# Performance work log

Hardware: AMD Instinct MI355X
Metric: run time of the kernel (lower is better)

Reference implementation:

```python
import jax, jax.numpy as jnp
import numpy as np

B, C, O, H, W, K, PAD = 8, 256, 256, 56, 56, 3, 1
KK = K * K


def setup_inputs() -> dict:
    key = jax.random.key(0)
    k1, k2, k3, k4 = jax.random.split(key, 4)
    x = jax.random.normal(k1, (B, C, H, W), jnp.float32)
    # offset conv params (original zero-inits; small random used so sampling is off-grid)
    w_off = jax.random.normal(k2, (2 * KK, C, K, K), jnp.float32) * 0.01
    b_off = jnp.zeros((2 * KK,), jnp.float32)
    # deformable conv weight/bias (torchvision DeformConv2d default has bias)
    w_dcn = jax.random.normal(k3, (O, C, K, K), jnp.float32) * (1.0 / np.sqrt(C * KK))
    b_dcn = jax.random.normal(k4, (O,), jnp.float32) * 0.01
    return dict(x=x, w_off=w_off, b_off=b_off, w_dcn=w_dcn, b_dcn=b_dcn)


def _conv3x3(x, w, b):
    y = jax.lax.conv_general_dilated(
        x, w, window_strides=(1, 1), padding=((PAD, PAD), (PAD, PAD)),
        dimension_numbers=('NCHW', 'OIHW', 'NCHW'))
    return y + b[None, :, None, None]


def _deform_sample(x, py, px):
    """Zero-padded bilinear gather of x[B,C,H,W] at (py,px)[B,KK,H,W] -> [B,C,KK,H,W]."""
    xf = x.reshape(B, C, H * W)
    y0 = jnp.floor(py)
    x0 = jnp.floor(px)
    fy = py - y0
    fx = px - x0
    val = 0.0
    for dy, dx, wgt in ((0, 0, (1 - fy) * (1 - fx)),
                        (0, 1, (1 - fy) * fx),
                        (1, 0, fy * (1 - fx)),
                        (1, 1, fy * fx)):
        yc = y0 + dy
        xc = x0 + dx
        ok = (yc >= 0) & (yc < H) & (xc >= 0) & (xc < W)  # zero-padding outside
        yi = jnp.clip(yc, 0, H - 1).astype(jnp.int32)
        xi = jnp.clip(xc, 0, W - 1).astype(jnp.int32)
        idx = (yi * W + xi).reshape(B, 1, KK * H * W)  # broadcast over channel dim
        g = jnp.take_along_axis(xf, idx, axis=2).reshape(B, C, KK, H, W)
        val = val + (wgt * ok)[:, None] * g
    return val


def reference(x, w_off, b_off, w_dcn, b_dcn):
    # 1) predict per-pixel offsets: [B, 2*K*K, H, W], torchvision layout (dy,dx) pairs
    off = _conv3x3(x, w_off, b_off)
    dy = off[:, 0::2]  # [B, KK, H, W]
    dx = off[:, 1::2]
    # 2) sampling grid: base pixel + kernel tap offset + learned offset
    ky = (jnp.arange(KK) // K - PAD).astype(jnp.float32)
    kx = (jnp.arange(KK) % K - PAD).astype(jnp.float32)
    hgrid = jnp.arange(H, dtype=jnp.float32)
    wgrid = jnp.arange(W, dtype=jnp.float32)
    py = hgrid[None, None, :, None] + ky[None, :, None, None] + dy
    px = wgrid[None, None, None, :] + kx[None, :, None, None] + dx
    # 3) bilinear gather + weighted accumulation over (c, kernel tap)
    val = _deform_sample(x, py, px)  # [B, C, KK, H, W]
    out = jnp.einsum('bckhw,ock->bohw', val, w_dcn.reshape(O, C, KK))
    return out + b_dcn[None, :, None, None]
```

## Files before the change

### kernel.cpp

```cpp
#include <hip/hip_runtime.h>

#define B_  8
#define C_  256
#define O_  256
#define H_  56
#define W_  56
#define HW_ 3136
#define KK_ 9
#define CK_ 2304
#define NKC 72

typedef __bf16    bf16x8 __attribute__((ext_vector_type(8)));
typedef float     f32x4  __attribute__((ext_vector_type(4)));

__device__ __forceinline__ int swz4(int r) { return (r & 3) ^ ((r >> 2) & 3); }

__device__ __forceinline__ float blo(unsigned u) {
    return __builtin_bit_cast(float, u << 16);
}
__device__ __forceinline__ float bhi(unsigned u) {
    return __builtin_bit_cast(float, u & 0xffff0000u);
}
__device__ __forceinline__ unsigned pkbf(float lo, float hi) {
    unsigned short a = __builtin_bit_cast(unsigned short, (__bf16)lo);
    unsigned short b = __builtin_bit_cast(unsigned short, (__bf16)hi);
    return (unsigned)a | ((unsigned)b << 16);
}

__device__ __forceinline__ uint4 bilin4(uint4 c00, uint4 c01, uint4 c10, uint4 c11,
                                        float4 wg) {
    uint4 o;
    float lo_, hi_;
    lo_ = wg.x*blo(c00.x) + wg.y*blo(c01.x) + wg.z*blo(c10.x) + wg.w*blo(c11.x);
    hi_ = wg.x*bhi(c00.x) + wg.y*bhi(c01.x) + wg.z*bhi(c10.x) + wg.w*bhi(c11.x);
    o.x = pkbf(lo_, hi_);
    lo_ = wg.x*blo(c00.y) + wg.y*blo(c01.y) + wg.z*blo(c10.y) + wg.w*blo(c11.y);
    hi_ = wg.x*bhi(c00.y) + wg.y*bhi(c01.y) + wg.z*bhi(c10.y) + wg.w*bhi(c11.y);
    o.y = pkbf(lo_, hi_);
    lo_ = wg.x*blo(c00.z) + wg.y*blo(c01.z) + wg.z*blo(c10.z) + wg.w*blo(c11.z);
    hi_ = wg.x*bhi(c00.z) + wg.y*bhi(c01.z) + wg.z*bhi(c10.z) + wg.w*bhi(c11.z);
    o.z = pkbf(lo_, hi_);
    lo_ = wg.x*blo(c00.w) + wg.y*blo(c01.w) + wg.z*blo(c10.w) + wg.w*blo(c11.w);
    hi_ = wg.x*bhi(c00.w) + wg.y*bhi(c01.w) + wg.z*bhi(c10.w) + wg.w*bhi(c11.w);
    o.w = pkbf(lo_, hi_);
    return o;
}

__global__ __launch_bounds__(256) void k_buildA(const float* __restrict__ w,
                                                unsigned short* __restrict__ wA) {
    int d  = blockIdx.x * 256 + threadIdx.x;
    int kc = d >> 13;
    int rd = d & 8191;
    int m  = rd >> 5;
    int pos = rd & 31;
    int q  = (pos >> 3) ^ swz4(m);
    int kl = q * 8 + (pos & 7);
    int gk = kc * 32 + kl;
    int tap = gk >> 8, c = gk & 255;
    __bf16 v = (__bf16)w[m * CK_ + c * KK_ + tap];
    wA[d] = __builtin_bit_cast(unsigned short, v);
}

__global__ __launch_bounds__(256) void k_transx(const float* __restrict__ x,
                                                unsigned short* __restrict__ xT) {
    __shared__ float s[64][65];
    int bt   = blockIdx.x;
    int c64  = bt & 3;
    int hw64 = (bt >> 2) % 49;
    int b    = bt / 196;
    int tx = threadIdx.x & 63;
    int ty = threadIdx.x >> 6;
#pragma unroll
    for (int i = 0; i < 16; ++i)
        s[i * 4 + ty][tx] =
            x[((size_t)(b * 256 + c64 * 64 + i * 4 + ty)) * HW_ + hw64 * 64 + tx];
    __syncthreads();
#pragma unroll
    for (int i = 0; i < 16; ++i) {
        float v = s[tx][i * 4 + ty];
        xT[((size_t)b * HW_ + hw64 * 64 + i * 4 + ty) * 256 + c64 * 64 + tx] =
            __builtin_bit_cast(unsigned short, (__bf16)v);
    }
}

__global__ __launch_bounds__(512) void k_offc1(const float* __restrict__ x,
                                               const float* __restrict__ w_off,
                                               float* __restrict__ part) {
    __shared__ float partial[8][64][18];
    int t  = threadIdx.x;
    int p  = t & 63;
    int cg = __builtin_amdgcn_readfirstlane(t >> 6);
    int orig = blockIdx.x;
    int blk  = (orig & 7) * 196 + (orig >> 3);
    int sl   = blk & 3;
    int un   = blk >> 2;
    int b    = un / 49;
    int pos0 = (un % 49) * 64;
    int pos  = pos0 + p;
    int h = pos / W_;
    int w = pos % W_;
    const float* xb = x + (size_t)b * C_ * HW_;

    float acc[18];
#pragma unroll
    for (int i = 0; i < 18; ++i) acc[i] = 0.f;

    for (int cc = 0; cc < 8; ++cc) {
        int c = sl * 64 + cg * 8 + cc;
        const float* xp = xb + c * HW_;
        float v[9];
#pragma unroll
        for (int dh = -1; dh <= 1; ++dh)
#pragma unroll
            for (int dw = -1; dw <= 1; ++dw) {
                int hh = h + dh, ww = w + dw;
                bool ok = (hh >= 0) & (hh < H_) & (ww >= 0) & (ww < W_);
                v[(dh + 1) * 3 + dw + 1] = ok ? xp[hh * W_ + ww] : 0.f;
            }
        const float* wc = w_off + c * KK_;
#pragma unroll
        for (int oc = 0; oc < 18; ++oc) {
            const float* wr = wc + oc * CK_;
#pragma unroll
            for (int k = 0; k < KK_; ++k)
                acc[oc] = fmaf(v[k], wr[k], acc[oc]);
        }
    }
#pragma unroll
    for (int oc = 0; oc < 18; ++oc) partial[cg][p][oc] = acc[oc];
    __syncthreads();

    float* po = part + (size_t)sl * (B_ * 18 * HW_);
    for (int e = t; e < 64 * 18; e += 512) {
        int oc = e >> 6;
        int pp = e & 63;
        float s = 0.f;
#pragma unroll
        for (int g = 0; g < 8; ++g) s += partial[g][pp][oc];
        po[((size_t)b * 18 + oc) * HW_ + pos0 + pp] = s;
    }
}

__global__ __launch_bounds__(256) void k_offc2(const float* __restrict__ part,
                                               const float* __restrict__ b_off,
                                               float* __restrict__ off) {
    int i = blockIdx.x * 256 + threadIdx.x;
    const int NP = B_ * 18 * HW_;
    int oc = (i / HW_) % 18;
    off[i] = part[i] + part[i + NP] + part[i + 2 * NP] + part[i + 3 * NP]
           + b_off[oc];
}

template<bool ISSUEC, bool ISSUEA, bool PROD, bool RELOAD>
__device__ __forceinline__ void fstage(
    int s, int chNext,
    const char* xb, const char* gA0,
    __bf16 (*s_b)[2048],
    int (*s_id)[64][4], float (*s_w)[64][4],
    int4& id, float4& wg,
    bf16x8 (&afUse)[4], bf16x8 (&afFill)[4],
    int aoffBase,
    int n, int tc, int sc, int lid, int quad, int swz,
    f32x4 (&acc)[4][4]) {

    if (RELOAD) {
        id = *(const int4*)s_id[(s + 1) >> 3][n];
        wg = *(const float4*)s_w[(s + 1) >> 3][n];
    }
    uint4 c0, c1, c2, c3;
    if (ISSUEC) {
        const char* p = xb + chNext * 64 + tc * 16;
        c0 = *(const uint4*)(p + id.x);
        c1 = *(const uint4*)(p + id.y);
        c2 = *(const uint4*)(p + id.z);
        c3 = *(const uint4*)(p + id.w);
    }
    if (ISSUEA) {
        const char* ga = gA0 + (size_t)(s + 1) * 16384 + aoffBase;
        afFill[0] = *(const bf16x8*)(ga);
        afFill[1] = *(const bf16x8*)(ga + 1024);
        afFill[2] = *(const bf16x8*)(ga + 2048);
        afFill[3] = *(const bf16x8*)(ga + 3072);
    }

    const bf16x8* pb = (const bf16x8*)s_b[s & 1];
    bf16x8 bv[4];
#pragma unroll
    for (int ni = 0; ni < 4; ++ni)
        bv[ni] = pb[(ni * 16 + lid) * 4 + (quad ^ swz)];

    __builtin_amdgcn_s_setprio(1);
#pragma unroll
    for (int mi = 0; mi < 4; ++mi)
#pragma unroll
        for (int ni = 0; ni < 4; ++ni)
            acc[mi][ni] = __builtin_amdgcn_mfma_f32_16x16x32_bf16(
                afUse[mi], bv[ni], acc[mi][ni], 0, 0, 0);
    __builtin_amdgcn_s_setprio(0);

    if (PROD) {
        uint4 o = bilin4(c0, c1, c2, c3, wg);
        *(uint4*)((char*)s_b[(s & 1) ^ 1] + n * 64 + sc * 16) = o;
    }
    asm volatile("s_waitcnt lgkmcnt(0)" ::: "memory");
    __builtin_amdgcn_s_barrier();
    __builtin_amdgcn_sched_barrier(0);
}

__global__ __launch_bounds__(256, 2) void k_fused(
    const unsigned short* __restrict__ xT,
    const float* __restrict__ off,
    const __bf16* __restrict__ wA,
    const float* __restrict__ b_dcn,
    float* __restrict__ out) {

    __shared__ __bf16 s_b[2][2048];
    __shared__ int    s_id[KK_][64][4];
    __shared__ float  s_w [KK_][64][4];

    int bid  = blockIdx.x;
    int g    = (bid & 7) * 49 + (bid >> 3);
    int b    = g / 49;
    int pos0 = (g % 49) * 64;
    int t    = threadIdx.x;
    int lane = t & 63;
    int wv   = t >> 6;
    int lid  = lane & 15;
    int quad = lane >> 4;
    int swz  = swz4(lid);

    for (int e = t; e < KK_ * 64; e += 256) {
        int k = e >> 6, n = e & 63;
        int pos = pos0 + n;
        int h = pos / W_, w = pos % W_;
        float dy = off[((size_t)b * 18 + 2 * k) * HW_ + pos];
        float dx = off[((size_t)b * 18 + 2 * k + 1) * HW_ + pos];
        float py = (float)(h + k / 3 - 1) + dy;
        float px = (float)(w + k % 3 - 1) + dx;
        float y0f = floorf(py), x0f = floorf(px);
        float fy = py - y0f, fx = px - x0f;
        int y0 = (int)y0f, x0 = (int)x0f;
        int y1 = y0 + 1,   x1 = x0 + 1;
        float oy0 = (y0 >= 0 && y0 < H_) ? 1.f : 0.f;
        float oy1 = (y1 >= 0 && y1 < H_) ? 1.f : 0.f;
        float ox0 = (x0 >= 0 && x0 < W_) ? 1.f : 0.f;
        float ox1 = (x1 >= 0 && x1 < W_) ? 1.f : 0.f;
        int y0c = min(max(y0, 0), H_ - 1), y1c = min(max(y1, 0), H_ - 1);
        int x0c = min(max(x0, 0), W_ - 1), x1c = min(max(x1, 0), W_ - 1);
        s_id[k][n][0] = (y0c * W_ + x0c) * 512;
        s_id[k][n][1] = (y0c * W_ + x1c) * 512;
        s_id[k][n][2] = (y1c * W_ + x0c) * 512;
        s_id[k][n][3] = (y1c * W_ + x1c) * 512;
        s_w[k][n][0] = (1.f - fy) * (1.f - fx) * oy0 * ox0;
        s_w[k][n][1] = (1.f - fy) * fx         * oy0 * ox1;
        s_w[k][n][2] = fy * (1.f - fx)         * oy1 * ox0;
        s_w[k][n][3] = fy * fx                 * oy1 * ox1;
    }
    __syncthreads();

    int n  = t >> 2;
    int tc = t & 3;
    int sc = tc ^ swz4(n);
    const char* xb  = (const char*)(xT + (size_t)b * HW_ * 256);
    const char* gA0 = (const char*)wA;
    int aoffBase = (wv * 64 + lid) * 64 + (quad ^ swz) * 16;

    f32x4 acc[4][4];
#pragma unroll
    for (int mi = 0; mi < 4; ++mi)
#pragma unroll
        for (int ni = 0; ni < 4; ++ni)
            acc[mi][ni] = (f32x4)(0.f);

    int4   id = *(const int4*)s_id[0][n];
    float4 wg = *(const float4*)s_w[0][n];
    bf16x8 afA[4], afB[4];

    {
        const char* p0 = xb + tc * 16;
        uint4 c0 = *(const uint4*)(p0 + id.x);
        uint4 c1 = *(const uint4*)(p0 + id.y);
        uint4 c2 = *(const uint4*)(p0 + id.z);
        uint4 c3 = *(const uint4*)(p0 + id.w);
        const char* ga = gA0 + aoffBase;
        afA[0] = *(const bf16x8*)(ga);
        afA[1] = *(const bf16x8*)(ga + 1024);
        afA[2] = *(const bf16x8*)(ga + 2048);
        afA[3] = *(const bf16x8*)(ga + 3072);
        uint4 o = bilin4(c0, c1, c2, c3, wg);
        *(uint4*)((char*)s_b[0] + n * 64 + sc * 16) = o;
    }
    asm volatile("s_waitcnt lgkmcnt(0)" ::: "memory");
    __builtin_amdgcn_s_barrier();
    __builtin_amdgcn_sched_barrier(0);

    for (int tap = 0; tap < 8; ++tap) {
        int s0 = tap * 8;
        fstage<true, true, true, false>(s0 + 0, 1, xb, gA0, s_b, s_id, s_w, id, wg, afA, afB, aoffBase, n, tc, sc, lid, quad, swz, acc);
        fstage<true, true, true, false>(s0 + 1, 2, xb, gA0, s_b, s_id, s_w, id, wg, afB, afA, aoffBase, n, tc, sc, lid, quad, swz, acc);
        fstage<true, true, true, false>(s0 + 2, 3, xb, gA0, s_b, s_id, s_w, id, wg, afA, afB, aoffBase, n, tc, sc, lid, quad, swz, acc);
        fstage<true, true, true, false>(s0 + 3, 4, xb, gA0, s_b, s_id, s_w, id, wg, afB, afA, aoffBase, n, tc, sc, lid, quad, swz, acc);
        fstage<true, true, true, false>(s0 + 4, 5, xb, gA0, s_b, s_id, s_w, id, wg, afA, afB, aoffBase, n, tc, sc, lid, quad, swz, acc);
        fstage<true, true, true, false>(s0 + 5, 6, xb, gA0, s_b, s_id, s_w, id, wg, afB, afA, aoffBase, n, tc, sc, lid, quad, swz, acc);
        fstage<true, true, true, false>(s0 + 6, 7, xb, gA0, s_b, s_id, s_w, id, wg, afA, afB, aoffBase, n, tc, sc, lid, quad, swz, acc);
        fstage<true, true, true, true >(s0 + 7, 0, xb, gA0, s_b, s_id, s_w, id, wg, afB, afA, aoffBase, n, tc, sc, lid, quad, swz, acc);
    }
    fstage<true,  true,  true,  false>(64, 1, xb, gA0, s_b, s_id, s_w, id, wg, afA, afB, aoffBase, n, tc, sc, lid, quad, swz, acc);
    fstage<true,  true,  true,  false>(65, 2, xb, gA0, s_b, s_id, s_w, id, wg, afB, afA, aoffBase, n, tc, sc, lid, quad, swz, acc);
    fstage<true,  true,  true,  false>(66, 3, xb, gA0, s_b, s_id, s_w, id, wg, afA, afB, aoffBase, n, tc, sc, lid, quad, swz, acc);
    fstage<true,  true,  true,  false>(67, 4, xb, gA0, s_b, s_id, s_w, id, wg, afB, afA, aoffBase, n, tc, sc, lid, quad, swz, acc);
    fstage<true,  true,  true,  false>(68, 5, xb, gA0, s_b, s_id, s_w, id, wg, afA, afB, aoffBase, n, tc, sc, lid, quad, swz, acc);
    fstage<true,  true,  true,  false>(69, 6, xb, gA0, s_b, s_id, s_w, id, wg, afB, afA, aoffBase, n, tc, sc, lid, quad, swz, acc);
    fstage<true,  true,  true,  false>(70, 7, xb, gA0, s_b, s_id, s_w, id, wg, afA, afB, aoffBase, n, tc, sc, lid, quad, swz, acc);
    fstage<false, false, false, false>(71, 0, xb, gA0, s_b, s_id, s_w, id, wg, afB, afA, aoffBase, n, tc, sc, lid, quad, swz, acc);

#pragma unroll
    for (int mi = 0; mi < 4; ++mi) {
#pragma unroll
        for (int r = 0; r < 4; ++r) {
            int m = wv * 64 + mi * 16 + quad * 4 + r;
            float bias = b_dcn[m];
            float* po = out + ((size_t)b * O_ + m) * HW_ + pos0 + lid;
#pragma unroll
            for (int ni = 0; ni < 4; ++ni)
                po[ni * 16] = acc[mi][ni][r] + bias;
        }
    }
}

extern "C" void kernel_launch(void* const* d_in, const int* in_sizes, int n_in,
                              void* d_out, int out_size, void* d_ws, size_t ws_size,
                              hipStream_t stream) {
    const float* x     = (const float*)d_in[0];
    const float* w_off = (const float*)d_in[1];
    const float* b_off = (const float*)d_in[2];
    const float* w_dcn = (const float*)d_in[3];
    const float* b_dcn = (const float*)d_in[4];
    float* out = (float*)d_out;

    const size_t offBytes  = (size_t)451584 * 4;
    const size_t wABytes   = (size_t)589824 * 2;
    const size_t xTBytes   = (size_t)B_ * HW_ * 256 * 2;
    float*          off  = (float*)d_ws;
    unsigned short* wA   = (unsigned short*)((char*)d_ws + offBytes);
    unsigned short* xT   = (unsigned short*)((char*)d_ws + offBytes + wABytes);
    float*          part = (float*)((char*)d_ws + offBytes + wABytes + xTBytes);

    k_buildA <<<2304, 256, 0, stream>>>(w_dcn, wA);
    k_transx <<<1568, 256, 0, stream>>>(x, xT);
    k_offc1  <<<1568, 512, 0, stream>>>(x, w_off, part);
    k_offc2  <<<1764, 256, 0, stream>>>(part, b_off, off);
    k_fused  <<<392,  256, 0, stream>>>(xT, off, (const __bf16*)wA, b_dcn, out);
}
```

Baseline: 193.8 us.

## Merge offset conv kernels and double K-step per pipeline stage in fused DCN

Drops the split-K offset convolution and its separate reduction kernel. One kernel now loops over all 256 channels per block and adds the bias directly, which removes the partial-sum buffer traffic and one launch, at the cost of fewer blocks (392) and more serial work per block. The fused deformable GEMM now handles two 64-channel chunks per pipeline stage (36 stages instead of 72). This halves the barriers and doubles the gather and A-fragment loads in flight, in exchange for higher register and LDS use.

```diff
diff --git a/kernel.cpp b/kernel.cpp
--- a/kernel.cpp
+++ b/kernel.cpp
@@ -83,19 +83,18 @@
     }
 }
 
-__global__ __launch_bounds__(512) void k_offc1(const float* __restrict__ x,
-                                               const float* __restrict__ w_off,
-                                               float* __restrict__ part) {
+__global__ __launch_bounds__(512) void k_offc(const float* __restrict__ x,
+                                              const float* __restrict__ w_off,
+                                              const float* __restrict__ b_off,
+                                              float* __restrict__ off) {
     __shared__ float partial[8][64][18];
     int t  = threadIdx.x;
     int p  = t & 63;
     int cg = __builtin_amdgcn_readfirstlane(t >> 6);
-    int orig = blockIdx.x;
-    int blk  = (orig & 7) * 196 + (orig >> 3);
-    int sl   = blk & 3;
-    int un   = blk >> 2;
-    int b    = un / 49;
-    int pos0 = (un % 49) * 64;
+    int bid  = blockIdx.x;
+    int g    = (bid & 7) * 49 + (bid >> 3);
+    int b    = g / 49;
+    int pos0 = (g % 49) * 64;
     int pos  = pos0 + p;
     int h = pos / W_;
     int w = pos % W_;
@@ -105,8 +104,8 @@
 #pragma unroll
     for (int i = 0; i < 18; ++i) acc[i] = 0.f;
 
-    for (int cc = 0; cc < 8; ++cc) {
-        int c = sl * 64 + cg * 8 + cc;
+    for (int cc = 0; cc < 32; ++cc) {
+        int c = cg * 32 + cc;
         const float* xp = xb + c * HW_;
         float v[9];
 #pragma unroll
@@ -130,77 +129,79 @@
     for (int oc = 0; oc < 18; ++oc) partial[cg][p][oc] = acc[oc];
     __syncthreads();
 
-    float* po = part + (size_t)sl * (B_ * 18 * HW_);
     for (int e = t; e < 64 * 18; e += 512) {
         int oc = e >> 6;
         int pp = e & 63;
         float s = 0.f;
 #pragma unroll
-        for (int g = 0; g < 8; ++g) s += partial[g][pp][oc];
-        po[((size_t)b * 18 + oc) * HW_ + pos0 + pp] = s;
-    }
-}
-
-__global__ __launch_bounds__(256) void k_offc2(const float* __restrict__ part,
-                                               const float* __restrict__ b_off,
-                                               float* __restrict__ off) {
-    int i = blockIdx.x * 256 + threadIdx.x;
-    const int NP = B_ * 18 * HW_;
-    int oc = (i / HW_) % 18;
-    off[i] = part[i] + part[i + NP] + part[i + 2 * NP] + part[i + 3 * NP]
-           + b_off[oc];
+        for (int gi = 0; gi < 8; ++gi) s += partial[gi][pp][oc];
+        off[((size_t)b * 18 + oc) * HW_ + pos0 + pp] = s + b_off[oc];
+    }
 }
 
 template<bool ISSUEC, bool ISSUEA, bool PROD, bool RELOAD>
 __device__ __forceinline__ void fstage(
-    int s, int chNext,
+    int s, int ch0, int ch1,
     const char* xb, const char* gA0,
-    __bf16 (*s_b)[2048],
+    __bf16 (*s_b)[2][2048],
     int (*s_id)[64][4], float (*s_w)[64][4],
     int4& id, float4& wg,
-    bf16x8 (&afUse)[4], bf16x8 (&afFill)[4],
+    bf16x8 (&afUse)[8], bf16x8 (&afFill)[8],
     int aoffBase,
     int n, int tc, int sc, int lid, int quad, int swz,
     f32x4 (&acc)[4][4]) {
 
     if (RELOAD) {
-        id = *(const int4*)s_id[(s + 1) >> 3][n];
-        wg = *(const float4*)s_w[(s + 1) >> 3][n];
-    }
-    uint4 c0, c1, c2, c3;
+        id = *(const int4*)s_id[(s + 1) >> 2][n];
+        wg = *(const float4*)s_w[(s + 1) >> 2][n];
+    }
+    uint4 c0, c1, c2, c3, c4, c5, c6, c7;
     if (ISSUEC) {
-        const char* p = xb + chNext * 64 + tc * 16;
-        c0 = *(const uint4*)(p + id.x);
-        c1 = *(const uint4*)(p + id.y);
-        c2 = *(const uint4*)(p + id.z);
-        c3 = *(const uint4*)(p + id.w);
+        const char* p0 = xb + ch0 * 64 + tc * 16;
+        c0 = *(const uint4*)(p0 + id.x);
+        c1 = *(const uint4*)(p0 + id.y);
+        c2 = *(const uint4*)(p0 + id.z);
+        c3 = *(const uint4*)(p0 + id.w);
+        const char* p1 = xb + ch1 * 64 + tc * 16;
+        c4 = *(const uint4*)(p1 + id.x);
+        c5 = *(const uint4*)(p1 + id.y);
+        c6 = *(const uint4*)(p1 + id.z);
+        c7 = *(const uint4*)(p1 + id.w);
     }
     if (ISSUEA) {
-        const char* ga = gA0 + (size_t)(s + 1) * 16384 + aoffBase;
+        const char* ga = gA0 + (size_t)(2 * (s + 1)) * 16384 + aoffBase;
         afFill[0] = *(const bf16x8*)(ga);
         afFill[1] = *(const bf16x8*)(ga + 1024);
         afFill[2] = *(const bf16x8*)(ga + 2048);
         afFill[3] = *(const bf16x8*)(ga + 3072);
-    }
-
-    const bf16x8* pb = (const bf16x8*)s_b[s & 1];
-    bf16x8 bv[4];
-#pragma unroll
-    for (int ni = 0; ni < 4; ++ni)
-        bv[ni] = pb[(ni * 16 + lid) * 4 + (quad ^ swz)];
+        afFill[4] = *(const bf16x8*)(ga + 16384);
+        afFill[5] = *(const bf16x8*)(ga + 16384 + 1024);
+        afFill[6] = *(const bf16x8*)(ga + 16384 + 2048);
+        afFill[7] = *(const bf16x8*)(ga + 16384 + 3072);
+    }
 
     __builtin_amdgcn_s_setprio(1);
 #pragma unroll
-    for (int mi = 0; mi < 4; ++mi)
+    for (int j = 0; j < 2; ++j) {
+        const bf16x8* pb = (const bf16x8*)s_b[s & 1][j];
+        bf16x8 bv[4];
 #pragma unroll
         for (int ni = 0; ni < 4; ++ni)
-            acc[mi][ni] = __builtin_amdgcn_mfma_f32_16x16x32_bf16(
-                afUse[mi], bv[ni], acc[mi][ni], 0, 0, 0);
+            bv[ni] = pb[(ni * 16 + lid) * 4 + (quad ^ swz)];
+#pragma unroll
+        for (int mi = 0; mi < 4; ++mi)
+#pragma unroll
+            for (int ni = 0; ni < 4; ++ni)
+                acc[mi][ni] = __builtin_amdgcn_mfma_f32_16x16x32_bf16(
+                    afUse[j * 4 + mi], bv[ni], acc[mi][ni], 0, 0, 0);
+    }
     __builtin_amdgcn_s_setprio(0);
 
     if (PROD) {
-        uint4 o = bilin4(c0, c1, c2, c3, wg);
-        *(uint4*)((char*)s_b[(s & 1) ^ 1] + n * 64 + sc * 16) = o;
+        uint4 o0 = bilin4(c0, c1, c2, c3, wg);
+        *(uint4*)((char*)s_b[(s & 1) ^ 1][0] + n * 64 + sc * 16) = o0;
+        uint4 o1 = bilin4(c4, c5, c6, c7, wg);
+        *(uint4*)((char*)s_b[(s & 1) ^ 1][1] + n * 64 + sc * 16) = o1;
     }
     asm volatile("s_waitcnt lgkmcnt(0)" ::: "memory");
     __builtin_amdgcn_s_barrier();
@@ -214,7 +215,7 @@
     const float* __restrict__ b_dcn,
     float* __restrict__ out) {
 
-    __shared__ __bf16 s_b[2][2048];
+    __shared__ __bf16 s_b[2][2][2048];
     __shared__ int    s_id[KK_][64][4];
     __shared__ float  s_w [KK_][64][4];
 
@@ -274,7 +275,7 @@
 
     int4   id = *(const int4*)s_id[0][n];
     float4 wg = *(const float4*)s_w[0][n];
-    bf16x8 afA[4], afB[4];
+    bf16x8 afA[8], afB[8];
 
     {
         const char* p0 = xb + tc * 16;
@@ -282,37 +283,40 @@
         uint4 c1 = *(const uint4*)(p0 + id.y);
         uint4 c2 = *(const uint4*)(p0 + id.z);
         uint4 c3 = *(const uint4*)(p0 + id.w);
+        const char* p1 = xb + 64 + tc * 16;
+        uint4 c4 = *(const uint4*)(p1 + id.x);
+        uint4 c5 = *(const uint4*)(p1 + id.y);
+        uint4 c6 = *(const uint4*)(p1 + id.z);
+        uint4 c7 = *(const uint4*)(p1 + id.w);
         const char* ga = gA0 + aoffBase;
         afA[0] = *(const bf16x8*)(ga);
         afA[1] = *(const bf16x8*)(ga + 1024);
         afA[2] = *(const bf16x8*)(ga + 2048);
         afA[3] = *(const bf16x8*)(ga + 3072);
-        uint4 o = bilin4(c0, c1, c2, c3, wg);
-        *(uint4*)((char*)s_b[0] + n * 64 + sc * 16) = o;
+        afA[4] = *(const bf16x8*)(ga + 16384);
+        afA[5] = *(const bf16x8*)(ga + 16384 + 1024);
+        afA[6] = *(const bf16x8*)(ga + 16384 + 2048);
+        afA[7] = *(const bf16x8*)(ga + 16384 + 3072);
+        uint4 o0 = bilin4(c0, c1, c2, c3, wg);
+        *(uint4*)((char*)s_b[0][0] + n * 64 + sc * 16) = o0;
+        uint4 o1 = bilin4(c4, c5, c6, c7, wg);
+        *(uint4*)((char*)s_b[0][1] + n * 64 + sc * 16) = o1;
     }
     asm volatile("s_waitcnt lgkmcnt(0)" ::: "memory");
     __builtin_amdgcn_s_barrier();
     __builtin_amdgcn_sched_barrier(0);
 
     for (int tap = 0; tap < 8; ++tap) {
-        int s0 = tap * 8;
-        fstage<true, true, true, false>(s0 + 0, 1, xb, gA0, s_b, s_id, s_w, id, wg, afA, afB, aoffBase, n, tc, sc, lid, quad, swz, acc);
-        fstage<true, true, true, false>(s0 + 1, 2, xb, gA0, s_b, s_id, s_w, id, wg, afB, afA, aoffBase, n, tc, sc, lid, quad, swz, acc);
-        fstage<true, true, true, false>(s0 + 2, 3, xb, gA0, s_b, s_id, s_w, id, wg, afA, afB, aoffBase, n, tc, sc, lid, quad, swz, acc);
-        fstage<true, true, true, false>(s0 + 3, 4, xb, gA0, s_b, s_id, s_w, id, wg, afB, afA, aoffBase, n, tc, sc, lid, quad, swz, acc);
-        fstage<true, true, true, false>(s0 + 4, 5, xb, gA0, s_b, s_id, s_w, id, wg, afA, afB, aoffBase, n, tc, sc, lid, quad, swz, acc);
-        fstage<true, true, true, false>(s0 + 5, 6, xb, gA0, s_b, s_id, s_w, id, wg, afB, afA, aoffBase, n, tc, sc, lid, quad, swz, acc);
-        fstage<true, true, true, false>(s0 + 6, 7, xb, gA0, s_b, s_id, s_w, id, wg, afA, afB, aoffBase, n, tc, sc, lid, quad, swz, acc);
-        fstage<true, true, true, true >(s0 + 7, 0, xb, gA0, s_b, s_id, s_w, id, wg, afB, afA, aoffBase, n, tc, sc, lid, quad, swz, acc);
-    }
-    fstage<true,  true,  true,  false>(64, 1, xb, gA0, s_b, s_id, s_w, id, wg, afA, afB, aoffBase, n, tc, sc, lid, quad, swz, acc);
-    fstage<true,  true,  true,  false>(65, 2, xb, gA0, s_b, s_id, s_w, id, wg, afB, afA, aoffBase, n, tc, sc, lid, quad, swz, acc);
-    fstage<true,  true,  true,  false>(66, 3, xb, gA0, s_b, s_id, s_w, id, wg, afA, afB, aoffBase, n, tc, sc, lid, quad, swz, acc);
-    fstage<true,  true,  true,  false>(67, 4, xb, gA0, s_b, s_id, s_w, id, wg, afB, afA, aoffBase, n, tc, sc, lid, quad, swz, acc);
-    fstage<true,  true,  true,  false>(68, 5, xb, gA0, s_b, s_id, s_w, id, wg, afA, afB, aoffBase, n, tc, sc, lid, quad, swz, acc);
-    fstage<true,  true,  true,  false>(69, 6, xb, gA0, s_b, s_id, s_w, id, wg, afB, afA, aoffBase, n, tc, sc, lid, quad, swz, acc);
-    fstage<true,  true,  true,  false>(70, 7, xb, gA0, s_b, s_id, s_w, id, wg, afA, afB, aoffBase, n, tc, sc, lid, quad, swz, acc);
-    fstage<false, false, false, false>(71, 0, xb, gA0, s_b, s_id, s_w, id, wg, afB, afA, aoffBase, n, tc, sc, lid, quad, swz, acc);
+        int s0 = tap * 4;
+        fstage<true, true, true, false>(s0 + 0, 2, 3, xb, gA0, s_b, s_id, s_w, id, wg, afA, afB, aoffBase, n, tc, sc, lid, quad, swz, acc);
+        fstage<true, true, true, false>(s0 + 1, 4, 5, xb, gA0, s_b, s_id, s_w, id, wg, afB, afA, aoffBase, n, tc, sc, lid, quad, swz, acc);
+        fstage<true, true, true, false>(s0 + 2, 6, 7, xb, gA0, s_b, s_id, s_w, id, wg, afA, afB, aoffBase, n, tc, sc, lid, quad, swz, acc);
+        fstage<true, true, true, true >(s0 + 3, 0, 1, xb, gA0, s_b, s_id, s_w, id, wg, afB, afA, aoffBase, n, tc, sc, lid, quad, swz, acc);
+    }
+    fstage<true,  true,  true,  false>(32, 2, 3, xb, gA0, s_b, s_id, s_w, id, wg, afA, afB, aoffBase, n, tc, sc, lid, quad, swz, acc);
+    fstage<true,  true,  true,  false>(33, 4, 5, xb, gA0, s_b, s_id, s_w, id, wg, afB, afA, aoffBase, n, tc, sc, lid, quad, swz, acc);
+    fstage<true,  true,  true,  false>(34, 6, 7, xb, gA0, s_b, s_id, s_w, id, wg, afA, afB, aoffBase, n, tc, sc, lid, quad, swz, acc);
+    fstage<false, false, false, false>(35, 0, 0, xb, gA0, s_b, s_id, s_w, id, wg, afB, afA, aoffBase, n, tc, sc, lid, quad, swz, acc);
 
 #pragma unroll
     for (int mi = 0; mi < 4; ++mi) {
@@ -340,15 +344,12 @@
 
     const size_t offBytes  = (size_t)451584 * 4;
     const size_t wABytes   = (size_t)589824 * 2;
-    const size_t xTBytes   = (size_t)B_ * HW_ * 256 * 2;
     float*          off  = (float*)d_ws;
     unsigned short* wA   = (unsigned short*)((char*)d_ws + offBytes);
     unsigned short* xT   = (unsigned short*)((char*)d_ws + offBytes + wABytes);
-    float*          part = (float*)((char*)d_ws + offBytes + wABytes + xTBytes);
 
     k_buildA <<<2304, 256, 0, stream>>>(w_dcn, wA);
     k_transx <<<1568, 256, 0, stream>>>(x, xT);
-    k_offc1  <<<1568, 512, 0, stream>>>(x, w_off, part);
-    k_offc2  <<<1764, 256, 0, stream>>>(part, b_off, off);
+    k_offc   <<<392,  512, 0, stream>>>(x, w_off, b_off, off);
     k_fused  <<<392,  256, 0, stream>>>(xT, off, (const __bf16*)wA, b_dcn, out);
 }
```

Result: no change. 192.3 us (-0.8%).
